# Kernel optimization log

Hardware: AMD Instinct MI355X
Metric: run time of the kernel (lower is better)

Reference implementation:

```python
import jax, jax.numpy as jnp
import numpy as np

N_NODES = 50000
N_EDGES = 400000
IN_DIM = 256
OUT_DIM = 64
HEADS = 2
ATTN_HIDDEN = 64
ALPHA = 0.2
TEMP = 0.55


def setup_inputs() -> dict:
    key = jax.random.key(0)
    k_x, k_src, k_dst, k_w, k_wa, k_a = jax.random.split(key, 6)
    x = jax.random.normal(k_x, (N_NODES, IN_DIM), dtype=jnp.float32)
    src = jax.random.randint(k_src, (N_EDGES,), 0, N_NODES, dtype=jnp.int32)
    dst = jnp.sort(jax.random.randint(k_dst, (N_EDGES,), 0, N_NODES, dtype=jnp.int32))
    # Glorot-uniform-like params
    def glorot(k, shape, fan_in, fan_out):
        lim = jnp.sqrt(6.0 / (fan_in + fan_out))
        return jax.random.uniform(k, shape, jnp.float32, -lim, lim)
    W = glorot(k_w, (IN_DIM, HEADS, OUT_DIM), IN_DIM, HEADS * OUT_DIM)
    W_attn = glorot(k_wa, (HEADS, 2 * OUT_DIM, ATTN_HIDDEN), 2 * OUT_DIM, ATTN_HIDDEN)
    a_vec = glorot(k_a, (HEADS, ATTN_HIDDEN), HEADS, ATTN_HIDDEN)
    return {"x": x, "W": W, "W_attn": W_attn, "a_vec": a_vec, "src": src, "dst": dst}


def reference(x, W, W_attn, a_vec, src, dst):
    N = x.shape[0]
    # node-level projection: [N, H, F]
    Wh = jnp.einsum('nd,dhf->nhf', x, W)
    # per-edge gathers
    Wh_src = Wh[src]                                   # [E, H, F]
    Wh_dst = Wh[dst]                                   # [E, H, F]
    z = jnp.concatenate([Wh_src, Wh_dst], axis=-1)     # [E, H, 2F]
    z_act = jax.nn.leaky_relu(jnp.einsum('ehf,hfc->ehc', z, W_attn), ALPHA)
    logits = jnp.einsum('ehc,hc->eh', z_act, a_vec).astype(jnp.float32) / TEMP
    # per-head segment softmax over incoming edges of each dst node
    seg_max = jax.ops.segment_max(logits, dst, num_segments=N)   # [N, H]
    ex = jnp.exp(logits - seg_max[dst])
    seg_sum = jax.ops.segment_sum(ex, dst, num_segments=N)
    alphas = (ex / (seg_sum[dst] + 1e-9)).astype(Wh_src.dtype)   # [E, H]
    # weighted scatter-sum of source messages
    out = jax.ops.segment_sum(Wh_src * alphas[..., None], dst, num_segments=N)  # [N, H, F]
    # concat=False -> mean over heads (dropout is identity at inference)
    return out.mean(axis=1)
```

## Files before the change

kernel.cpp:

```cpp
#include <hip/hip_runtime.h>
#include <hip/hip_bf16.h>
#include <math.h>

#define N_NODES 50000
#define N_EDGES 400000
#define IN_DIM 256
#define OUT_DIM 64
#define HEADS 2
#define ATTN_HIDDEN 64
#define ALPHA_SLOPE 0.2f
#define TEMP 0.55f
#define NHF 128
#define ZDIM 384

typedef __bf16 bf16x8 __attribute__((ext_vector_type(8)));
typedef float f32x4 __attribute__((ext_vector_type(4)));

__device__ __forceinline__ ushort f2bf(float f) {
    unsigned u = __float_as_uint(f);
    u = (u + 0x7fffu + ((u >> 16) & 1u)) >> 16;
    return (ushort)u;
}
__device__ __forceinline__ unsigned pack2(float a, float b) {
    return (unsigned)f2bf(a) | ((unsigned)f2bf(b) << 16);
}
__device__ __forceinline__ float bfl(unsigned u) { return __uint_as_float(u << 16); }
__device__ __forceinline__ float bfh(unsigned u) { return __uint_as_float(u & 0xffff0000u); }

__global__ __launch_bounds__(256) void k_combine(const float* __restrict__ W,
                                                 const float* __restrict__ Wa,
                                                 ushort* __restrict__ Wctf,
                                                 const int* __restrict__ dst,
                                                 int* __restrict__ seg) {
    __shared__ float col[64];
    const int b = blockIdx.x;
    const int t = threadIdx.x;
    if (b >= ZDIM) {
        int n = (b - ZDIM) * 256 + t;
        if (n > N_NODES) return;
        int lo = 0, hi = N_EDGES;
        while (lo < hi) {
            int mid = (lo + hi) >> 1;
            if (dst[mid] < n) lo = mid + 1; else hi = mid;
        }
        seg[n] = lo;
        return;
    }
    const int n = b;
    const int k = t;
    const int c = n >> 4, r16 = n & 15;
    const int kc = k >> 5, q = (k >> 3) & 3, j = k & 7;
    const size_t pos = (size_t)(((c * 8 + kc) * 64 + q * 16 + r16)) * 8 + j;

    float val;
    if (n < 128) {
        val = W[(size_t)k * NHF + n];
    } else {
        const int part = (n - 128) >> 7;
        const int idx = (n - 128) & 127;
        const int h = idx >> 6;
        const int cc = idx & 63;
        const int fb = part ? 64 : 0;
        if (t < 64) col[t] = Wa[(size_t)h * 8192 + (size_t)(fb + t) * 64 + cc];
        __syncthreads();
        const float* wr = W + (size_t)k * NHF + h * 64;
        float acc = 0.f;
#pragma unroll
        for (int f = 0; f < 64; f++) acc += wr[f] * col[f];
        val = acc;
    }
    Wctf[pos] = f2bf(val);
}

__global__ __launch_bounds__(256, 3) void k_gemm(const float* __restrict__ x,
                                                 const ushort* __restrict__ Wctf,
                                                 ushort* __restrict__ Zb) {
    const int t = threadIdx.x;
    const int w = t >> 6, lane = t & 63;
    const int q = lane >> 4, r16 = lane & 15;
    const int chalf = (w & 1) * 12;
    const int rowbase = blockIdx.x * 64 + (w >> 1) * 32;
    if (rowbase >= N_NODES) return;

    int rA0 = rowbase + r16;
    int rA1 = rowbase + 16 + r16;
    rA0 = rA0 < N_NODES ? rA0 : N_NODES - 1;
    rA1 = rA1 < N_NODES ? rA1 : N_NODES - 1;
    const float* xp0 = x + (size_t)rA0 * IN_DIM + q * 8;
    const float* xp1 = x + (size_t)rA1 * IN_DIM + q * 8;
    const ushort* bp = Wctf + chalf * 4096 + lane * 8;

    f32x4 acc[2][12];
#pragma unroll
    for (int mt = 0; mt < 2; mt++)
#pragma unroll
        for (int c = 0; c < 12; c++) acc[mt][c] = (f32x4){0.f, 0.f, 0.f, 0.f};

#pragma unroll 1
    for (int kc = 0; kc < 8; kc++) {
        const float4 a00 = *(const float4*)(xp0 + kc * 32);
        const float4 a01 = *(const float4*)(xp0 + kc * 32 + 4);
        const float4 a10 = *(const float4*)(xp1 + kc * 32);
        const float4 a11 = *(const float4*)(xp1 + kc * 32 + 4);
        uint4 p0, p1;
        p0.x = pack2(a00.x, a00.y); p0.y = pack2(a00.z, a00.w);
        p0.z = pack2(a01.x, a01.y); p0.w = pack2(a01.z, a01.w);
        p1.x = pack2(a10.x, a10.y); p1.y = pack2(a10.z, a10.w);
        p1.z = pack2(a11.x, a11.y); p1.w = pack2(a11.z, a11.w);
        const bf16x8 af0 = *(const bf16x8*)&p0;
        const bf16x8 af1 = *(const bf16x8*)&p1;
        const ushort* bk = bp + kc * 512;
#pragma unroll
        for (int c = 0; c < 12; c++) {
            const bf16x8 bf = *(const bf16x8*)(bk + c * 4096);
            acc[0][c] = __builtin_amdgcn_mfma_f32_16x16x32_bf16(af0, bf, acc[0][c], 0, 0, 0);
            acc[1][c] = __builtin_amdgcn_mfma_f32_16x16x32_bf16(af1, bf, acc[1][c], 0, 0, 0);
        }
    }
#pragma unroll
    for (int mt = 0; mt < 2; mt++)
#pragma unroll
        for (int c = 0; c < 12; c++)
#pragma unroll
            for (int rr = 0; rr < 4; rr++) {
                const int row = rowbase + mt * 16 + q * 4 + rr;
                if (row < N_NODES)
                    Zb[(size_t)row * ZDIM + (chalf + c) * 16 + r16] = f2bf(acc[mt][c][rr]);
            }
}

__global__ __launch_bounds__(256) void k_fused(const ushort* __restrict__ Zb,
                                               const float* __restrict__ avec,
                                               const int* __restrict__ src,
                                               const int* __restrict__ seg,
                                               float* __restrict__ out) {
    const int lane = threadIdx.x & 63;
    const int wv = threadIdx.x >> 6;
    const int g = lane >> 4, l16 = lane & 15;
    const int n = blockIdx.x * 16 + wv * 4 + g;
    if (n >= N_NODES) return;
    const int choff = 8 * l16;

    const float4 af0 = *(const float4*)(avec + choff);
    const float4 af1 = *(const float4*)(avec + choff + 4);
    const float a[8] = {af0.x, af0.y, af0.z, af0.w, af1.x, af1.y, af1.z, af1.w};

    const uint4 udv = *(const uint4*)(Zb + (size_t)n * ZDIM + 256 + choff);
    const float ud[8] = {bfl(udv.x), bfh(udv.x), bfl(udv.y), bfh(udv.y),
                         bfl(udv.z), bfh(udv.z), bfl(udv.w), bfh(udv.w)};

    const int e0 = seg[n], e1 = seg[n + 1];
    const int cnt = e1 - e0;
    float m = -INFINITY, l = 0.f;
    float acc[8] = {0.f, 0.f, 0.f, 0.f, 0.f, 0.f, 0.f, 0.f};

    auto step = [&](const uint4 cus, const uint4 cwh) {
        float p;
        {
            float v0, v1, s0, s1;
            v0 = bfl(cus.x) + ud[0]; v1 = bfh(cus.x) + ud[1];
            s0 = fmaxf(v0, ALPHA_SLOPE * v0); s1 = fmaxf(v1, ALPHA_SLOPE * v1);
            p = s0 * a[0] + s1 * a[1];
            v0 = bfl(cus.y) + ud[2]; v1 = bfh(cus.y) + ud[3];
            s0 = fmaxf(v0, ALPHA_SLOPE * v0); s1 = fmaxf(v1, ALPHA_SLOPE * v1);
            p += s0 * a[2] + s1 * a[3];
            v0 = bfl(cus.z) + ud[4]; v1 = bfh(cus.z) + ud[5];
            s0 = fmaxf(v0, ALPHA_SLOPE * v0); s1 = fmaxf(v1, ALPHA_SLOPE * v1);
            p += s0 * a[4] + s1 * a[5];
            v0 = bfl(cus.w) + ud[6]; v1 = bfh(cus.w) + ud[7];
            s0 = fmaxf(v0, ALPHA_SLOPE * v0); s1 = fmaxf(v1, ALPHA_SLOPE * v1);
            p += s0 * a[6] + s1 * a[7];
        }
        p += __shfl_xor(p, 1, 64);
        p += __shfl_xor(p, 2, 64);
        p += __shfl_xor(p, 4, 64);
        const float logit = p * (1.0f / TEMP);
        const float nm = fmaxf(m, logit);
        const float sc = __expf(m - nm);
        const float wgt = __expf(logit - nm);
        l = l * sc + wgt;
        acc[0] = acc[0] * sc + wgt * bfl(cwh.x);
        acc[1] = acc[1] * sc + wgt * bfh(cwh.x);
        acc[2] = acc[2] * sc + wgt * bfl(cwh.y);
        acc[3] = acc[3] * sc + wgt * bfh(cwh.y);
        acc[4] = acc[4] * sc + wgt * bfl(cwh.z);
        acc[5] = acc[5] * sc + wgt * bfh(cwh.z);
        acc[6] = acc[6] * sc + wgt * bfl(cwh.w);
        acc[7] = acc[7] * sc + wgt * bfh(cwh.w);
        m = nm;
    };

    uint4 us0 = make_uint4(0,0,0,0), wh0 = us0, us1 = us0, wh1 = us0;
    if (cnt > 0) {
        const int s = src[e0];
        us0 = *(const uint4*)(Zb + (size_t)s * ZDIM + 128 + choff);
        wh0 = *(const uint4*)(Zb + (size_t)s * ZDIM + choff);
    }
    if (cnt > 1) {
        const int s = src[e0 + 1];
        us1 = *(const uint4*)(Zb + (size_t)s * ZDIM + 128 + choff);
        wh1 = *(const uint4*)(Zb + (size_t)s * ZDIM + choff);
    }
    int i = 0;
    while (i < cnt) {
        {
            const uint4 cus = us0, cwh = wh0;
            if (i + 2 < cnt) {
                const int sn = src[e0 + i + 2];
                us0 = *(const uint4*)(Zb + (size_t)sn * ZDIM + 128 + choff);
                wh0 = *(const uint4*)(Zb + (size_t)sn * ZDIM + choff);
            }
            step(cus, cwh);
        }
        if (++i >= cnt) break;
        {
            const uint4 cus = us1, cwh = wh1;
            if (i + 2 < cnt) {
                const int sn = src[e0 + i + 2];
                us1 = *(const uint4*)(Zb + (size_t)sn * ZDIM + 128 + choff);
                wh1 = *(const uint4*)(Zb + (size_t)sn * ZDIM + choff);
            }
            step(cus, cwh);
        }
        ++i;
    }

    const float inv = 0.5f / (l + 1e-9f);
#pragma unroll
    for (int j = 0; j < 8; j++) {
        const float v = acc[j] * inv;
        acc[j] = v + __shfl_xor(v, 8, 64);
    }
    if (l16 < 8) {
        float4 o0 = make_float4(acc[0], acc[1], acc[2], acc[3]);
        float4 o1 = make_float4(acc[4], acc[5], acc[6], acc[7]);
        float* op = out + (size_t)n * 64 + choff;
        *(float4*)op = o0;
        *(float4*)(op + 4) = o1;
    }
}

extern "C" void kernel_launch(void* const* d_in, const int* in_sizes, int n_in,
                              void* d_out, int out_size, void* d_ws, size_t ws_size,
                              hipStream_t stream) {
    const float* x    = (const float*)d_in[0];
    const float* W    = (const float*)d_in[1];
    const float* Wa   = (const float*)d_in[2];
    const float* avec = (const float*)d_in[3];
    const int*   src  = (const int*)d_in[4];
    const int*   dst  = (const int*)d_in[5];
    float* out = (float*)d_out;

    ushort* Zb   = (ushort*)d_ws;
    ushort* Wctf = Zb + 19200000;
    int*    seg  = (int*)((char*)d_ws + 38596608);

    const int seg_blocks = (N_NODES + 1 + 255) / 256;
    k_combine <<<ZDIM + seg_blocks, 256, 0, stream>>>(W, Wa, Wctf, dst, seg);
    k_gemm    <<<(N_NODES + 63) / 64, 256, 0, stream>>>(x, Wctf, Zb);
    k_fused   <<<(N_NODES + 15) / 16, 256, 0, stream>>>(Zb, avec, src, seg, out);
}
```

Baseline: 174.9 us.

## Software-pipeline GEMM operand loads and split softmax into two independent chains

The projection GEMM now keeps its B fragments and next x tile in registers, prefetching the following k-chunk while MFMAs run on the current one, so global load latency overlaps compute. In the edge kernel, the online-softmax recurrence is split into two independent running states (max, sum, accumulator) over alternating edges, merged at the end. This breaks the serial exp/max dependency chain to raise ILP. Both changes raise register pressure, which can reduce occupancy.

Result: slower. 208.5 us (+19.2%).

```diff
diff --git a/kernel.cpp b/kernel.cpp
--- a/kernel.cpp
+++ b/kernel.cpp
@@ -92,16 +92,19 @@
 
     f32x4 acc[2][12];
 #pragma unroll
-    for (int mt = 0; mt < 2; mt++)
-#pragma unroll
-        for (int c = 0; c < 12; c++) acc[mt][c] = (f32x4){0.f, 0.f, 0.f, 0.f};
+    for (int c = 0; c < 12; c++) { acc[0][c] = (f32x4){0.f,0.f,0.f,0.f}; acc[1][c] = (f32x4){0.f,0.f,0.f,0.f}; }
+
+    float4 a00 = *(const float4*)(xp0);
+    float4 a01 = *(const float4*)(xp0 + 4);
+    float4 a10 = *(const float4*)(xp1);
+    float4 a11 = *(const float4*)(xp1 + 4);
+    uint4 b[12];
+#pragma unroll
+    for (int c = 0; c < 12; c++) b[c] = *(const uint4*)(bp + c * 4096);
 
 #pragma unroll 1
     for (int kc = 0; kc < 8; kc++) {
-        const float4 a00 = *(const float4*)(xp0 + kc * 32);
-        const float4 a01 = *(const float4*)(xp0 + kc * 32 + 4);
-        const float4 a10 = *(const float4*)(xp1 + kc * 32);
-        const float4 a11 = *(const float4*)(xp1 + kc * 32 + 4);
+        const int kn = ((kc + 1) & 7) * 32;
         uint4 p0, p1;
         p0.x = pack2(a00.x, a00.y); p0.y = pack2(a00.z, a00.w);
         p0.z = pack2(a01.x, a01.y); p0.w = pack2(a01.z, a01.w);
@@ -109,12 +112,17 @@
         p1.z = pack2(a11.x, a11.y); p1.w = pack2(a11.z, a11.w);
         const bf16x8 af0 = *(const bf16x8*)&p0;
         const bf16x8 af1 = *(const bf16x8*)&p1;
-        const ushort* bk = bp + kc * 512;
+        a00 = *(const float4*)(xp0 + kn);
+        a01 = *(const float4*)(xp0 + kn + 4);
+        a10 = *(const float4*)(xp1 + kn);
+        a11 = *(const float4*)(xp1 + kn + 4);
+        const ushort* bkn = bp + kn * 16;
 #pragma unroll
         for (int c = 0; c < 12; c++) {
-            const bf16x8 bf = *(const bf16x8*)(bk + c * 4096);
+            const bf16x8 bf = *(const bf16x8*)&b[c];
             acc[0][c] = __builtin_amdgcn_mfma_f32_16x16x32_bf16(af0, bf, acc[0][c], 0, 0, 0);
             acc[1][c] = __builtin_amdgcn_mfma_f32_16x16x32_bf16(af1, bf, acc[1][c], 0, 0, 0);
+            b[c] = *(const uint4*)(bkn + c * 4096);
         }
     }
 #pragma unroll
@@ -151,10 +159,11 @@
 
     const int e0 = seg[n], e1 = seg[n + 1];
     const int cnt = e1 - e0;
-    float m = -INFINITY, l = 0.f;
-    float acc[8] = {0.f, 0.f, 0.f, 0.f, 0.f, 0.f, 0.f, 0.f};
-
-    auto step = [&](const uint4 cus, const uint4 cwh) {
+
+    float m0 = -INFINITY, l0 = 0.f, m1 = -INFINITY, l1 = 0.f;
+    float ac0[8] = {0,0,0,0,0,0,0,0}, ac1[8] = {0,0,0,0,0,0,0,0};
+
+    auto step = [&](float& m, float& l, float* ac, const uint4 cus, const uint4 cwh) {
         float p;
         {
             float v0, v1, s0, s1;
@@ -179,14 +188,14 @@
         const float sc = __expf(m - nm);
         const float wgt = __expf(logit - nm);
         l = l * sc + wgt;
-        acc[0] = acc[0] * sc + wgt * bfl(cwh.x);
-        acc[1] = acc[1] * sc + wgt * bfh(cwh.x);
-        acc[2] = acc[2] * sc + wgt * bfl(cwh.y);
-        acc[3] = acc[3] * sc + wgt * bfh(cwh.y);
-        acc[4] = acc[4] * sc + wgt * bfl(cwh.z);
-        acc[5] = acc[5] * sc + wgt * bfh(cwh.z);
-        acc[6] = acc[6] * sc + wgt * bfl(cwh.w);
-        acc[7] = acc[7] * sc + wgt * bfh(cwh.w);
+        ac[0] = ac[0] * sc + wgt * bfl(cwh.x);
+        ac[1] = ac[1] * sc + wgt * bfh(cwh.x);
+        ac[2] = ac[2] * sc + wgt * bfl(cwh.y);
+        ac[3] = ac[3] * sc + wgt * bfh(cwh.y);
+        ac[4] = ac[4] * sc + wgt * bfl(cwh.z);
+        ac[5] = ac[5] * sc + wgt * bfh(cwh.z);
+        ac[6] = ac[6] * sc + wgt * bfl(cwh.w);
+        ac[7] = ac[7] * sc + wgt * bfh(cwh.w);
         m = nm;
     };
 
@@ -202,33 +211,33 @@
         wh1 = *(const uint4*)(Zb + (size_t)s * ZDIM + choff);
     }
     int i = 0;
-    while (i < cnt) {
-        {
-            const uint4 cus = us0, cwh = wh0;
-            if (i + 2 < cnt) {
-                const int sn = src[e0 + i + 2];
-                us0 = *(const uint4*)(Zb + (size_t)sn * ZDIM + 128 + choff);
-                wh0 = *(const uint4*)(Zb + (size_t)sn * ZDIM + choff);
-            }
-            step(cus, cwh);
-        }
-        if (++i >= cnt) break;
-        {
-            const uint4 cus = us1, cwh = wh1;
-            if (i + 2 < cnt) {
-                const int sn = src[e0 + i + 2];
-                us1 = *(const uint4*)(Zb + (size_t)sn * ZDIM + 128 + choff);
-                wh1 = *(const uint4*)(Zb + (size_t)sn * ZDIM + choff);
-            }
-            step(cus, cwh);
-        }
-        ++i;
-    }
-
-    const float inv = 0.5f / (l + 1e-9f);
+    while (i + 1 < cnt) {
+        const uint4 cu0 = us0, cw0 = wh0, cu1 = us1, cw1 = wh1;
+        if (i + 2 < cnt) {
+            const int s = src[e0 + i + 2];
+            us0 = *(const uint4*)(Zb + (size_t)s * ZDIM + 128 + choff);
+            wh0 = *(const uint4*)(Zb + (size_t)s * ZDIM + choff);
+        }
+        if (i + 3 < cnt) {
+            const int s = src[e0 + i + 3];
+            us1 = *(const uint4*)(Zb + (size_t)s * ZDIM + 128 + choff);
+            wh1 = *(const uint4*)(Zb + (size_t)s * ZDIM + choff);
+        }
+        step(m0, l0, ac0, cu0, cw0);
+        step(m1, l1, ac1, cu1, cw1);
+        i += 2;
+    }
+    if (i < cnt) step(m0, l0, ac0, us0, wh0);
+
+    const float mm = fmaxf(m0, m1);
+    const float s0 = (m0 != -INFINITY) ? __expf(m0 - mm) : 0.f;
+    const float s1 = (m1 != -INFINITY) ? __expf(m1 - mm) : 0.f;
+    const float lt = l0 * s0 + l1 * s1;
+    const float inv = 0.5f / (lt + 1e-9f);
+    float acc[8];
 #pragma unroll
     for (int j = 0; j < 8; j++) {
-        const float v = acc[j] * inv;
+        const float v = (ac0[j] * s0 + ac1[j] * s1) * inv;
         acc[j] = v + __shfl_xor(v, 8, 64);
     }
     if (l16 < 8) {
```
